# Performance work log

Measured on AMD Instinct MI355X. Metric: run time of the kernel, lower is better.

The kernel has to match this reference:

```python
import jax, jax.numpy as jnp
import numpy as np

ORDER = 2
BN_EPS = 1e-5

def setup_inputs() -> dict:
    key = jax.random.key(0)
    ks = jax.random.split(key, 8)
    B, N, L, H = 32, 512, 12, 64
    S = 2                      # support_len
    OUT = 64                   # out_dim
    M = ORDER * S * H          # einsum middle dim = 256
    x = jax.random.normal(ks[0], (B, N, L, H), dtype=jnp.float32)
    # row-scaled random diffusion matrices to keep multi-hop propagation stable
    support = jax.random.uniform(ks[1], (S, N, N), dtype=jnp.float32) / N
    scale = 1.0 / M
    weight = scale * jax.random.normal(ks[2], (L, M, OUT), dtype=jnp.float32)
    eps = jnp.zeros((1,), dtype=jnp.float32)
    gamma = jnp.ones((OUT,), dtype=jnp.float32)
    beta = jnp.zeros((OUT,), dtype=jnp.float32)
    w2 = jax.random.normal(ks[3], (OUT, OUT), dtype=jnp.float32) / np.sqrt(OUT)
    b2 = jnp.zeros((OUT,), dtype=jnp.float32)
    return {"x": x, "support": support, "weight": weight, "eps": eps,
            "gamma": gamma, "beta": beta, "w2": w2, "b2": b2}

def reference(x, support, weight, eps, gamma, beta, w2, b2):
    B, N, L, H = x.shape
    xv = x.reshape(B, N, L * H)            # [B,N,LH]
    res = []
    for i in range(support.shape[0]):      # small fixed loop over supports
        A = support[i]                     # [N,N]
        out = xv
        for _ in range(ORDER):
            out = (1.0 + eps) * out + jnp.einsum('nm,bmd->bnd', A, out)
            res.append(out)
    out = jnp.stack(res, axis=-1)          # [B,N,LH,K], K = order*support_len
    K = out.shape[-1]
    out = out.reshape(B, N, L, H * K)      # [B,N,L,M]
    out = jnp.einsum('bnlm,lmo->bno', out, weight)   # [B,N,OUT]
    # dropout is identity in eval mode
    C = out.shape[-1]
    flat = out.reshape(B * N, C)
    mean = flat.mean(axis=0)
    var = flat.var(axis=0)                 # biased, matching torch BN training
    normed = (flat - mean) * jax.lax.rsqrt(var + BN_EPS) * gamma + beta
    y = jax.nn.relu(normed.reshape(B, N, C))
    return jnp.einsum('bnc,oc->bno', y, w2) + b2
```

## Files before the change

kernel.cpp:

```cpp
#include <hip/hip_runtime.h>
#include <hip/hip_bf16.h>
#include <cstddef>
#include <cstdint>

#define B_   32
#define N_   512
#define D_   768
#define OUT_ 64
#define R_   (B_ * N_)

typedef unsigned short u16;
typedef __bf16 bf16x8 __attribute__((ext_vector_type(8)));
typedef float  f32x4  __attribute__((ext_vector_type(4)));
typedef unsigned short u16x8 __attribute__((ext_vector_type(8)));

__device__ __forceinline__ u16 f2bf(float f) {
    __hip_bfloat16 h = __float2bfloat16(f);
    return __builtin_bit_cast(u16, h);
}

__device__ __forceinline__ f32x4 mfma16(u16x8 a, u16x8 b, f32x4 c) {
    return __builtin_amdgcn_mfma_f32_16x16x32_bf16(
        __builtin_bit_cast(bf16x8, a), __builtin_bit_cast(bf16x8, b), c, 0, 0, 0);
}

__device__ __forceinline__ void gl2lds16(const void* g, void* l) {
    __builtin_amdgcn_global_load_lds(
        (const __attribute__((address_space(1))) unsigned int*)g,
        (__attribute__((address_space(3))) unsigned int*)l, 16, 0, 0);
}

__global__ __launch_bounds__(256) void cast_x(
    const float* __restrict__ x, u16* __restrict__ xb)
{
    int i = (blockIdx.x * 256 + threadIdx.x) * 8;
    f32x4 a = *(const f32x4*)(x + i);
    f32x4 b = *(const f32x4*)(x + i + 4);
    u16x8 o;
#pragma unroll
    for (int j = 0; j < 4; ++j) { o[j] = f2bf(a[j]); o[4 + j] = f2bf(b[j]); }
    *(u16x8*)(xb + i) = o;
}

__global__ __launch_bounds__(256) void build_M(
    const float* __restrict__ support, const float* __restrict__ epsp,
    u16* __restrict__ Mall, u16* __restrict__ MT)
{
    __shared__ float t[32][33];
    const int tid = threadIdx.x;
    const int s = blockIdx.z, n0 = blockIdx.y * 32, m0 = blockIdx.x * 32;
    const float f = 1.0f + epsp[0];
    const float* S = support + (size_t)s * 262144;
#pragma unroll
    for (int p = 0; p < 4; ++p) {
        int nl = p * 8 + (tid >> 5), ml = tid & 31;
        float v = S[(size_t)(n0 + nl) * 512 + m0 + ml];
        if (n0 + nl == m0 + ml) v += f;
        Mall[(size_t)s * 524288 + (size_t)(n0 + nl) * 512 + m0 + ml] = f2bf(v);
        t[nl][ml] = v;
    }
    __syncthreads();
#pragma unroll
    for (int p = 0; p < 4; ++p) {
        int ml = p * 8 + (tid >> 5), nl = tid & 31;
        MT[(size_t)s * 262144 + (size_t)(m0 + ml) * 512 + n0 + nl] = f2bf(t[nl][ml]);
    }
}

__global__ __launch_bounds__(256) void build_Wt(
    const float* __restrict__ w, u16* __restrict__ Wt)
{
    int idx = blockIdx.x * 256 + threadIdx.x;
    int k = idx / 49152, rem = idx % 49152;
    int o = rem / 768, d = rem % 768;
    int l = d >> 6, hh = d & 63;
    Wt[idx] = f2bf(w[((size_t)l * 256 + hh * 4 + k) * 64 + o]);
}

__global__ __launch_bounds__(256) void msq(
    const u16* __restrict__ Mall_in, const u16* __restrict__ MT,
    u16* __restrict__ Mall_out)
{
    __shared__ __align__(16) u16 sm[8192];
    u16* Ps = sm; u16* Qs = sm + 4096;
    const int tid = threadIdx.x, lane = tid & 63, wid = tid >> 6;
    const int wr = wid >> 1, wc = wid & 1;
    const int s = blockIdx.z, i0 = blockIdx.y * 128, j0 = blockIdx.x * 128;
    const u16* A = Mall_in + (size_t)s * 524288;
    const u16* Bq = MT + (size_t)s * 262144;
    const int lrow = lane & 15, lk = (lane >> 4) * 8;

    const u16* gsrc[4]; u16* ldst[4];
#pragma unroll
    for (int t = 0; t < 4; ++t) {
        int idx = wid * 4 + t;
        if (idx < 8) { gsrc[t] = A  + (size_t)(i0 + idx * 16 + lrow) * 512 + lk; ldst[t] = Ps + idx * 512; }
        else { int s2 = idx - 8; gsrc[t] = Bq + (size_t)(j0 + s2 * 16 + lrow) * 512 + lk; ldst[t] = Qs + s2 * 512; }
    }
    f32x4 acc[4][4] = {};
    for (int k0 = 0; k0 < 512; k0 += 32) {
#pragma unroll
        for (int t = 0; t < 4; ++t) gl2lds16(gsrc[t], ldst[t]);
#pragma unroll
        for (int t = 0; t < 4; ++t) gsrc[t] += 32;
        __syncthreads();
        u16x8 af[4], bq[4];
#pragma unroll
        for (int f = 0; f < 4; ++f) af[f] = *(const u16x8*)(Ps + (wr * 4 + f) * 512 + lane * 8);
#pragma unroll
        for (int f = 0; f < 4; ++f) bq[f] = *(const u16x8*)(Qs + (wc * 4 + f) * 512 + lane * 8);
#pragma unroll
        for (int fi = 0; fi < 4; ++fi)
#pragma unroll
            for (int fj = 0; fj < 4; ++fj) acc[fi][fj] = mfma16(af[fi], bq[fj], acc[fi][fj]);
        __syncthreads();
    }
    const int q = lane >> 4;
    u16* Co = Mall_out + (size_t)s * 524288 + 262144;
#pragma unroll
    for (int fi = 0; fi < 4; ++fi)
#pragma unroll
        for (int fj = 0; fj < 4; ++fj)
#pragma unroll
            for (int r = 0; r < 4; ++r) {
                int n = i0 + wr * 64 + fi * 16 + q * 4 + r;
                int c = j0 + wc * 64 + fj * 16 + lrow;
                Co[(size_t)n * 512 + c] = f2bf(acc[fi][fj][r]);
            }
}

__global__ __launch_bounds__(256) void zgemm(
    const u16* __restrict__ Wt, const u16* __restrict__ xb, u16* __restrict__ Z)
{
    __shared__ __align__(16) char smem[4 * 9216];
    u16* Ps = (u16*)smem;
    u16* Qs = (u16*)(smem + 8192);
    const int tid = threadIdx.x, lane = tid & 63, wid = tid >> 6;
    const int wr = wid >> 1, wc = wid & 1;
    const int j0 = blockIdx.x * 128, i0 = blockIdx.y * 128;
    const int lrow = lane & 15, lk = (lane >> 4) * 8;

    const u16* gsrc[4]; u16* ldst[4];
#pragma unroll
    for (int t = 0; t < 4; ++t) {
        int idx = wid * 4 + t;
        if (idx < 8) { gsrc[t] = Wt + (size_t)(i0 + idx * 16 + lrow) * 768 + lk; ldst[t] = Ps + idx * 512; }
        else { int s2 = idx - 8; gsrc[t] = xb + (size_t)(j0 + s2 * 16 + lrow) * 768 + lk; ldst[t] = Qs + s2 * 512; }
    }
    f32x4 acc[4][4] = {};
    for (int k0 = 0; k0 < 768; k0 += 32) {
#pragma unroll
        for (int t = 0; t < 4; ++t) gl2lds16(gsrc[t], ldst[t]);
#pragma unroll
        for (int t = 0; t < 4; ++t) gsrc[t] += 32;
        __syncthreads();
        u16x8 af[4], bq[4];
#pragma unroll
        for (int f = 0; f < 4; ++f) af[f] = *(const u16x8*)(Ps + (wr * 4 + f) * 512 + lane * 8);
#pragma unroll
        for (int f = 0; f < 4; ++f) bq[f] = *(const u16x8*)(Qs + (wc * 4 + f) * 512 + lane * 8);
#pragma unroll
        for (int fi = 0; fi < 4; ++fi)
#pragma unroll
            for (int fj = 0; fj < 4; ++fj) acc[fi][fj] = mfma16(af[fi], bq[fj], acc[fi][fj]);
        __syncthreads();
    }
    u16* Rw = (u16*)(smem + wid * 9216);
    const int q = lane >> 4;
#pragma unroll
    for (int fi = 0; fi < 4; ++fi)
#pragma unroll
        for (int fj = 0; fj < 4; ++fj)
#pragma unroll
            for (int r = 0; r < 4; ++r)
                Rw[(fi * 16 + q * 4 + r) * 72 + fj * 16 + lrow] = f2bf(acc[fi][fj][r]);
    __syncthreads();
    const int kq = blockIdx.y * 2 + wr;
    const int b  = j0 >> 9;
    const int m0 = (j0 & 511) + wc * 64;
#pragma unroll
    for (int p = 0; p < 8; ++p) {
        int row = p * 8 + (lane >> 3);
        int cc  = (lane & 7) * 8;
        u16x8 v = *(const u16x8*)(Rw + row * 72 + cc);
        *(u16x8*)(Z + ((size_t)(kq * 32 + b) * 64 + row) * 512 + m0 + cc) = v;
    }
}

__global__ __launch_bounds__(256) void ygemm(
    const u16* __restrict__ Mall, const u16* __restrict__ Z, float* __restrict__ Y1)
{
    __shared__ __align__(16) u16 sm[10240];
    u16* As_ = sm; u16* Bs_ = sm + 8192;
    const int tid = threadIdx.x, lane = tid & 63, wid = tid >> 6;
    const int n0 = blockIdx.x * 256, kb = blockIdx.y;
    const int k = kb >> 5;
    const u16* Ak  = Mall + (size_t)k * 262144;
    const u16* Zkb = Z + (size_t)kb * 64 * 512;
    const int lrow = lane & 15, lk = (lane >> 4) * 8;

    const u16* gsrc[5]; u16* ldst[5];
#pragma unroll
    for (int t = 0; t < 5; ++t) {
        int idx = wid * 5 + t;
        if (idx < 16) { gsrc[t] = Ak + (size_t)(n0 + idx * 16 + lrow) * 512 + lk; ldst[t] = As_ + idx * 512; }
        else { int s2 = idx - 16; gsrc[t] = Zkb + (size_t)(s2 * 16 + lrow) * 512 + lk; ldst[t] = Bs_ + s2 * 512; }
    }
    f32x4 acc[4][4] = {};
    for (int k0 = 0; k0 < 512; k0 += 32) {
#pragma unroll
        for (int t = 0; t < 5; ++t) gl2lds16(gsrc[t], ldst[t]);
#pragma unroll
        for (int t = 0; t < 5; ++t) gsrc[t] += 32;
        __syncthreads();
        u16x8 af[4], bq[4];
#pragma unroll
        for (int f = 0; f < 4; ++f) af[f] = *(const u16x8*)(As_ + (wid * 4 + f) * 512 + lane * 8);
#pragma unroll
        for (int f = 0; f < 4; ++f) bq[f] = *(const u16x8*)(Bs_ + f * 512 + lane * 8);
#pragma unroll
        for (int fi = 0; fi < 4; ++fi)
#pragma unroll
            for (int fj = 0; fj < 4; ++fj) acc[fi][fj] = mfma16(af[fi], bq[fj], acc[fi][fj]);
        __syncthreads();
    }
    const int q = lane >> 4;
    float* Yb = Y1 + (size_t)kb * 512 * 64;
#pragma unroll
    for (int fi = 0; fi < 4; ++fi)
#pragma unroll
        for (int fj = 0; fj < 4; ++fj)
#pragma unroll
            for (int r = 0; r < 4; ++r) {
                int n = n0 + wid * 64 + fi * 16 + q * 4 + r;
                int o = fj * 16 + lrow;
                Yb[(size_t)n * 64 + o] = acc[fi][fj][r];
            }
}

__global__ __launch_bounds__(256) void bn_part(
    const float* __restrict__ Y1, float* __restrict__ part)
{
    const int blk = blockIdx.x, tid = threadIdx.x;
    const int o = tid & 63, g = tid >> 6;
    float s = 0.f, s2 = 0.f;
    for (int r = blk * 64 + g; r < blk * 64 + 64; r += 4) {
        float v = 0.f;
#pragma unroll
        for (int k = 0; k < 4; ++k) v += Y1[((size_t)(k << 14) + r) * 64 + o];
        s += v; s2 += v * v;
    }
    __shared__ float ls[4][64], ls2[4][64];
    ls[g][o] = s; ls2[g][o] = s2;
    __syncthreads();
    if (tid < 64) {
        float t = 0.f, t2 = 0.f;
#pragma unroll
        for (int g2 = 0; g2 < 4; ++g2) { t += ls[g2][tid]; t2 += ls2[g2][tid]; }
        part[blk * 128 + tid]      = t;
        part[blk * 128 + 64 + tid] = t2;
    }
}

__global__ __launch_bounds__(256) void bn_final(
    const float* __restrict__ part, float* __restrict__ stats)
{
    const int tid = threadIdx.x;
    const int c = tid & 63, g = tid >> 6;
    float s = 0.f, s2 = 0.f;
    for (int b = g; b < 256; b += 4) {
        s  += part[b * 128 + c];
        s2 += part[b * 128 + 64 + c];
    }
    __shared__ float ls[4][64], ls2[4][64];
    ls[g][c] = s; ls2[g][c] = s2;
    __syncthreads();
    if (tid < 64) {
        float t = 0.f, t2 = 0.f;
#pragma unroll
        for (int g2 = 0; g2 < 4; ++g2) { t += ls[g2][tid]; t2 += ls2[g2][tid]; }
        float mean = t * (1.0f / R_);
        float var  = t2 * (1.0f / R_) - mean * mean;
        stats[tid]      = mean;
        stats[64 + tid] = rsqrtf(var + 1e-5f);
    }
}

__global__ __launch_bounds__(256) void bn_out(
    const float* __restrict__ Y1, const float* __restrict__ stats,
    const float* __restrict__ gamma, const float* __restrict__ beta,
    const float* __restrict__ w2, const float* __restrict__ b2,
    float* __restrict__ out)
{
    __shared__ float ys[64 * 68];
    __shared__ float w2s[64 * 65];
    __shared__ float mn[64], rs[64], ga[64], be[64], bb[64];
    const int tid = threadIdx.x;
    const int r0 = blockIdx.x * 64;
#pragma unroll
    for (int i = 0; i < 16; ++i) {
        int idx = tid + i * 256;
        w2s[(idx >> 6) * 65 + (idx & 63)] = w2[idx];
    }
    if (tid < 64) {
        mn[tid] = stats[tid]; rs[tid] = stats[64 + tid];
        ga[tid] = gamma[tid]; be[tid] = beta[tid]; bb[tid] = b2[tid];
    }
    __syncthreads();
    const int o = tid & 63, rg = tid >> 6;
#pragma unroll
    for (int p = 0; p < 16; ++p) {
        int rl = p * 4 + rg;
        int r = r0 + rl;
        float v = 0.f;
#pragma unroll
        for (int k = 0; k < 4; ++k) v += Y1[((size_t)(k << 14) + r) * 64 + o];
        v = (v - mn[o]) * rs[o] * ga[o] + be[o];
        ys[o * 68 + rl] = fmaxf(v, 0.f);
    }
    __syncthreads();
    const int ol = tid & 63, rg2 = tid >> 6;
    float acc[16];
#pragma unroll
    for (int j = 0; j < 16; ++j) acc[j] = bb[ol];
    for (int c = 0; c < 64; ++c) {
        float wv = w2s[ol * 65 + c];
        const float* yr = ys + c * 68 + rg2 * 16;
        f32x4 y0 = *(const f32x4*)(yr);
        f32x4 y1 = *(const f32x4*)(yr + 4);
        f32x4 y2 = *(const f32x4*)(yr + 8);
        f32x4 y3 = *(const f32x4*)(yr + 12);
#pragma unroll
        for (int j = 0; j < 4; ++j) {
            acc[j]      = fmaf(wv, y0[j], acc[j]);
            acc[4 + j]  = fmaf(wv, y1[j], acc[4 + j]);
            acc[8 + j]  = fmaf(wv, y2[j], acc[8 + j]);
            acc[12 + j] = fmaf(wv, y3[j], acc[12 + j]);
        }
    }
#pragma unroll
    for (int j = 0; j < 16; ++j)
        out[(size_t)(r0 + rg2 * 16 + j) * OUT_ + ol] = acc[j];
}

extern "C" void kernel_launch(void* const* d_in, const int* in_sizes, int n_in,
                              void* d_out, int out_size, void* d_ws, size_t ws_size,
                              hipStream_t stream)
{
    const float* x       = (const float*)d_in[0];
    const float* support = (const float*)d_in[1];
    const float* weight  = (const float*)d_in[2];
    const float* eps     = (const float*)d_in[3];
    const float* gamma   = (const float*)d_in[4];
    const float* beta    = (const float*)d_in[5];
    const float* w2      = (const float*)d_in[6];
    const float* b2      = (const float*)d_in[7];
    float* out = (float*)d_out;

    char* ws = (char*)d_ws;
    u16*   xb    = (u16*)(ws);
    u16*   Mall  = (u16*)(ws + 25165824);
    u16*   MT    = (u16*)(ws + 27262976);
    u16*   Wt    = (u16*)(ws + 28311552);
    u16*   Z     = (u16*)(ws + 28704768);
    float* Y1    = (float*)(ws + 37093376);
    float* part  = (float*)(ws + 53870592);
    float* stats = (float*)(ws + 54001664);

    cast_x  <<<6144,            256, 0, stream>>>(x, xb);
    build_M <<<dim3(16, 16, 2), 256, 0, stream>>>(support, eps, Mall, MT);
    build_Wt<<<768,             256, 0, stream>>>(weight, Wt);
    msq     <<<dim3(4, 4, 2),   256, 0, stream>>>(Mall, MT, Mall);
    zgemm   <<<dim3(128, 2),    256, 0, stream>>>(Wt, xb, Z);
    ygemm   <<<dim3(2, 128),    256, 0, stream>>>(Mall, Z, Y1);
    bn_part <<<256,             256, 0, stream>>>(Y1, part);
    bn_final<<<1,               256, 0, stream>>>(part, stats);
    bn_out  <<<256,             256, 0, stream>>>(Y1, stats, gamma, beta, w2, b2, out);
}
```

Before: 192.1 us.

## Fuse prep kernels, interleave M powers, and sum K terms inside Y GEMM

Merges the three preprocessing kernels into a single launch. Stores the support-power matrices in an interleaved [N, K*N] layout and the Z intermediate in [B*64, K*N], so each wave of the new ysum kernel handles one hop term. The four partial results are then reduced in LDS, which drops the 4x fp32 Y1 buffer. ysum also emits the BN partial sums, removing the bn_part kernel and the later re-read of Y1, at the cost of smaller per-wave tiles and more LDS per block.

```diff
diff --git a/kernel.cpp b/kernel.cpp
--- a/kernel.cpp
+++ b/kernel.cpp
@@ -30,72 +30,68 @@
         (__attribute__((address_space(3))) unsigned int*)l, 16, 0, 0);
 }
 
-__global__ __launch_bounds__(256) void cast_x(
-    const float* __restrict__ x, u16* __restrict__ xb)
-{
-    int i = (blockIdx.x * 256 + threadIdx.x) * 8;
-    f32x4 a = *(const f32x4*)(x + i);
-    f32x4 b = *(const f32x4*)(x + i + 4);
-    u16x8 o;
-#pragma unroll
-    for (int j = 0; j < 4; ++j) { o[j] = f2bf(a[j]); o[4 + j] = f2bf(b[j]); }
-    *(u16x8*)(xb + i) = o;
-}
-
-__global__ __launch_bounds__(256) void build_M(
-    const float* __restrict__ support, const float* __restrict__ epsp,
-    u16* __restrict__ Mall, u16* __restrict__ MT)
-{
+__global__ __launch_bounds__(256) void prep(
+    const float* __restrict__ x, const float* __restrict__ support,
+    const float* __restrict__ weight, const float* __restrict__ epsp,
+    u16* __restrict__ xb, u16* __restrict__ MallC, u16* __restrict__ MT,
+    u16* __restrict__ Wt)
+{
+    const int blk = blockIdx.x, tid = threadIdx.x;
     __shared__ float t[32][33];
-    const int tid = threadIdx.x;
-    const int s = blockIdx.z, n0 = blockIdx.y * 32, m0 = blockIdx.x * 32;
-    const float f = 1.0f + epsp[0];
-    const float* S = support + (size_t)s * 262144;
-#pragma unroll
-    for (int p = 0; p < 4; ++p) {
-        int nl = p * 8 + (tid >> 5), ml = tid & 31;
-        float v = S[(size_t)(n0 + nl) * 512 + m0 + ml];
-        if (n0 + nl == m0 + ml) v += f;
-        Mall[(size_t)s * 524288 + (size_t)(n0 + nl) * 512 + m0 + ml] = f2bf(v);
-        t[nl][ml] = v;
-    }
-    __syncthreads();
-#pragma unroll
-    for (int p = 0; p < 4; ++p) {
-        int ml = p * 8 + (tid >> 5), nl = tid & 31;
-        MT[(size_t)s * 262144 + (size_t)(m0 + ml) * 512 + n0 + nl] = f2bf(t[nl][ml]);
-    }
-}
-
-__global__ __launch_bounds__(256) void build_Wt(
-    const float* __restrict__ w, u16* __restrict__ Wt)
-{
-    int idx = blockIdx.x * 256 + threadIdx.x;
-    int k = idx / 49152, rem = idx % 49152;
-    int o = rem / 768, d = rem % 768;
-    int l = d >> 6, hh = d & 63;
-    Wt[idx] = f2bf(w[((size_t)l * 256 + hh * 4 + k) * 64 + o]);
+    if (blk < 6144) {
+        int i = (blk * 256 + tid) * 8;
+        f32x4 a = *(const f32x4*)(x + i);
+        f32x4 b = *(const f32x4*)(x + i + 4);
+        u16x8 o;
+#pragma unroll
+        for (int j = 0; j < 4; ++j) { o[j] = f2bf(a[j]); o[4 + j] = f2bf(b[j]); }
+        *(u16x8*)(xb + i) = o;
+    } else if (blk < 6656) {
+        int local = blk - 6144;
+        int s = local >> 8, rem = local & 255;
+        int n0 = (rem >> 4) * 32, m0 = (rem & 15) * 32;
+        const float f = 1.0f + epsp[0];
+        const float* S = support + (size_t)s * 262144;
+#pragma unroll
+        for (int p = 0; p < 4; ++p) {
+            int nl = p * 8 + (tid >> 5), ml = tid & 31;
+            float v = S[(size_t)(n0 + nl) * 512 + m0 + ml];
+            if (n0 + nl == m0 + ml) v += f;
+            MallC[(size_t)(n0 + nl) * 2048 + s * 1024 + m0 + ml] = f2bf(v);
+            t[nl][ml] = v;
+        }
+        __syncthreads();
+#pragma unroll
+        for (int p = 0; p < 4; ++p) {
+            int ml = p * 8 + (tid >> 5), nl = tid & 31;
+            MT[(size_t)s * 262144 + (size_t)(m0 + ml) * 512 + n0 + nl] = f2bf(t[nl][ml]);
+        }
+    } else {
+        int idx = (blk - 6656) * 256 + tid;
+        int k = idx / 49152, rem = idx % 49152;
+        int o = rem / 768, d = rem % 768;
+        int l = d >> 6, hh = d & 63;
+        Wt[idx] = f2bf(weight[((size_t)l * 256 + hh * 4 + k) * 64 + o]);
+    }
 }
 
 __global__ __launch_bounds__(256) void msq(
-    const u16* __restrict__ Mall_in, const u16* __restrict__ MT,
-    u16* __restrict__ Mall_out)
+    const u16* __restrict__ MallC_in, const u16* __restrict__ MT,
+    u16* __restrict__ MallC_out)
 {
     __shared__ __align__(16) u16 sm[8192];
     u16* Ps = sm; u16* Qs = sm + 4096;
     const int tid = threadIdx.x, lane = tid & 63, wid = tid >> 6;
     const int wr = wid >> 1, wc = wid & 1;
     const int s = blockIdx.z, i0 = blockIdx.y * 128, j0 = blockIdx.x * 128;
-    const u16* A = Mall_in + (size_t)s * 524288;
-    const u16* Bq = MT + (size_t)s * 262144;
     const int lrow = lane & 15, lk = (lane >> 4) * 8;
 
     const u16* gsrc[4]; u16* ldst[4];
 #pragma unroll
     for (int t = 0; t < 4; ++t) {
         int idx = wid * 4 + t;
-        if (idx < 8) { gsrc[t] = A  + (size_t)(i0 + idx * 16 + lrow) * 512 + lk; ldst[t] = Ps + idx * 512; }
-        else { int s2 = idx - 8; gsrc[t] = Bq + (size_t)(j0 + s2 * 16 + lrow) * 512 + lk; ldst[t] = Qs + s2 * 512; }
+        if (idx < 8) { gsrc[t] = MallC_in + (size_t)(i0 + idx * 16 + lrow) * 2048 + s * 1024 + lk; ldst[t] = Ps + idx * 512; }
+        else { int s2 = idx - 8; gsrc[t] = MT + (size_t)s * 262144 + (size_t)(j0 + s2 * 16 + lrow) * 512 + lk; ldst[t] = Qs + s2 * 512; }
     }
     f32x4 acc[4][4] = {};
     for (int k0 = 0; k0 < 512; k0 += 32) {
@@ -116,7 +112,6 @@
         __syncthreads();
     }
     const int q = lane >> 4;
-    u16* Co = Mall_out + (size_t)s * 524288 + 262144;
 #pragma unroll
     for (int fi = 0; fi < 4; ++fi)
 #pragma unroll
@@ -125,140 +120,143 @@
             for (int r = 0; r < 4; ++r) {
                 int n = i0 + wr * 64 + fi * 16 + q * 4 + r;
                 int c = j0 + wc * 64 + fj * 16 + lrow;
-                Co[(size_t)n * 512 + c] = f2bf(acc[fi][fj][r]);
+                MallC_out[(size_t)n * 2048 + (2 * s + 1) * 512 + c] = f2bf(acc[fi][fj][r]);
             }
 }
 
 __global__ __launch_bounds__(256) void zgemm(
     const u16* __restrict__ Wt, const u16* __restrict__ xb, u16* __restrict__ Z)
 {
-    __shared__ __align__(16) char smem[4 * 9216];
-    u16* Ps = (u16*)smem;
-    u16* Qs = (u16*)(smem + 8192);
+    __shared__ __align__(16) u16 sm[9216];
+    u16* As = sm; u16* Bs = sm + 2048;
     const int tid = threadIdx.x, lane = tid & 63, wid = tid >> 6;
     const int wr = wid >> 1, wc = wid & 1;
-    const int j0 = blockIdx.x * 128, i0 = blockIdx.y * 128;
+    const int j0 = blockIdx.x * 128, k = blockIdx.y;
+    const int b = j0 >> 9, m0 = j0 & 511;
     const int lrow = lane & 15, lk = (lane >> 4) * 8;
 
-    const u16* gsrc[4]; u16* ldst[4];
-#pragma unroll
-    for (int t = 0; t < 4; ++t) {
-        int idx = wid * 4 + t;
-        if (idx < 8) { gsrc[t] = Wt + (size_t)(i0 + idx * 16 + lrow) * 768 + lk; ldst[t] = Ps + idx * 512; }
-        else { int s2 = idx - 8; gsrc[t] = xb + (size_t)(j0 + s2 * 16 + lrow) * 768 + lk; ldst[t] = Qs + s2 * 512; }
-    }
-    f32x4 acc[4][4] = {};
+    const u16* gsrc[3]; u16* ldst[3];
+#pragma unroll
+    for (int t = 0; t < 3; ++t) {
+        int idx = wid * 3 + t;
+        if (idx < 4) { gsrc[t] = Wt + (size_t)(k * 64 + idx * 16 + lrow) * 768 + lk; ldst[t] = As + idx * 512; }
+        else { int s2 = idx - 4; gsrc[t] = xb + (size_t)(j0 + s2 * 16 + lrow) * 768 + lk; ldst[t] = Bs + s2 * 512; }
+    }
+    f32x4 acc[2][4] = {};
     for (int k0 = 0; k0 < 768; k0 += 32) {
 #pragma unroll
-        for (int t = 0; t < 4; ++t) gl2lds16(gsrc[t], ldst[t]);
-#pragma unroll
-        for (int t = 0; t < 4; ++t) gsrc[t] += 32;
-        __syncthreads();
-        u16x8 af[4], bq[4];
-#pragma unroll
-        for (int f = 0; f < 4; ++f) af[f] = *(const u16x8*)(Ps + (wr * 4 + f) * 512 + lane * 8);
-#pragma unroll
-        for (int f = 0; f < 4; ++f) bq[f] = *(const u16x8*)(Qs + (wc * 4 + f) * 512 + lane * 8);
-#pragma unroll
-        for (int fi = 0; fi < 4; ++fi)
+        for (int t = 0; t < 3; ++t) gl2lds16(gsrc[t], ldst[t]);
+#pragma unroll
+        for (int t = 0; t < 3; ++t) gsrc[t] += 32;
+        __syncthreads();
+        u16x8 af[2], bq[4];
+#pragma unroll
+        for (int f = 0; f < 2; ++f) af[f] = *(const u16x8*)(As + (wr * 2 + f) * 512 + lane * 8);
+#pragma unroll
+        for (int f = 0; f < 4; ++f) bq[f] = *(const u16x8*)(Bs + (wc * 4 + f) * 512 + lane * 8);
+#pragma unroll
+        for (int fi = 0; fi < 2; ++fi)
 #pragma unroll
             for (int fj = 0; fj < 4; ++fj) acc[fi][fj] = mfma16(af[fi], bq[fj], acc[fi][fj]);
         __syncthreads();
     }
-    u16* Rw = (u16*)(smem + wid * 9216);
+    u16* Rw = sm + wid * 2304;
     const int q = lane >> 4;
 #pragma unroll
-    for (int fi = 0; fi < 4; ++fi)
+    for (int fi = 0; fi < 2; ++fi)
 #pragma unroll
         for (int fj = 0; fj < 4; ++fj)
 #pragma unroll
             for (int r = 0; r < 4; ++r)
                 Rw[(fi * 16 + q * 4 + r) * 72 + fj * 16 + lrow] = f2bf(acc[fi][fj][r]);
     __syncthreads();
-    const int kq = blockIdx.y * 2 + wr;
-    const int b  = j0 >> 9;
-    const int m0 = (j0 & 511) + wc * 64;
-#pragma unroll
-    for (int p = 0; p < 8; ++p) {
+#pragma unroll
+    for (int p = 0; p < 4; ++p) {
         int row = p * 8 + (lane >> 3);
-        int cc  = (lane & 7) * 8;
+        int cc = (lane & 7) * 8;
+        int o = wr * 32 + row;
         u16x8 v = *(const u16x8*)(Rw + row * 72 + cc);
-        *(u16x8*)(Z + ((size_t)(kq * 32 + b) * 64 + row) * 512 + m0 + cc) = v;
-    }
-}
-
-__global__ __launch_bounds__(256) void ygemm(
-    const u16* __restrict__ Mall, const u16* __restrict__ Z, float* __restrict__ Y1)
-{
-    __shared__ __align__(16) u16 sm[10240];
-    u16* As_ = sm; u16* Bs_ = sm + 8192;
+        *(u16x8*)(Z + ((size_t)(b * 64 + o) * 4 + k) * 512 + m0 + wc * 64 + cc) = v;
+    }
+}
+
+__global__ __launch_bounds__(256) void ysum(
+    const u16* __restrict__ MallC, const u16* __restrict__ Z,
+    float* __restrict__ Ysum, float* __restrict__ part)
+{
+    __shared__ __align__(16) char smem[43520];
+    u16*   St = (u16*)smem;
+    float* Rk = (float*)smem;
+    float* vs = (float*)(smem + 34816);
     const int tid = threadIdx.x, lane = tid & 63, wid = tid >> 6;
-    const int n0 = blockIdx.x * 256, kb = blockIdx.y;
-    const int k = kb >> 5;
-    const u16* Ak  = Mall + (size_t)k * 262144;
-    const u16* Zkb = Z + (size_t)kb * 64 * 512;
+    const int n0 = blockIdx.x * 32, b = blockIdx.y;
     const int lrow = lane & 15, lk = (lane >> 4) * 8;
 
-    const u16* gsrc[5]; u16* ldst[5];
-#pragma unroll
-    for (int t = 0; t < 5; ++t) {
-        int idx = wid * 5 + t;
-        if (idx < 16) { gsrc[t] = Ak + (size_t)(n0 + idx * 16 + lrow) * 512 + lk; ldst[t] = As_ + idx * 512; }
-        else { int s2 = idx - 16; gsrc[t] = Zkb + (size_t)(s2 * 16 + lrow) * 512 + lk; ldst[t] = Bs_ + s2 * 512; }
-    }
-    f32x4 acc[4][4] = {};
+    const u16* gsrc[6]; u16* ldst[6];
+#pragma unroll
+    for (int t = 0; t < 2; ++t) {
+        gsrc[t] = MallC + (size_t)(n0 + t * 16 + lrow) * 2048 + wid * 512 + lk;
+        ldst[t] = St + (wid * 6 + t) * 512;
+    }
+#pragma unroll
+    for (int t = 0; t < 4; ++t) {
+        gsrc[2 + t] = Z + (size_t)(b * 64 + t * 16 + lrow) * 2048 + wid * 512 + lk;
+        ldst[2 + t] = St + (wid * 6 + 2 + t) * 512;
+    }
+    f32x4 acc[2][4] = {};
     for (int k0 = 0; k0 < 512; k0 += 32) {
 #pragma unroll
-        for (int t = 0; t < 5; ++t) gl2lds16(gsrc[t], ldst[t]);
-#pragma unroll
-        for (int t = 0; t < 5; ++t) gsrc[t] += 32;
-        __syncthreads();
-        u16x8 af[4], bq[4];
-#pragma unroll
-        for (int f = 0; f < 4; ++f) af[f] = *(const u16x8*)(As_ + (wid * 4 + f) * 512 + lane * 8);
-#pragma unroll
-        for (int f = 0; f < 4; ++f) bq[f] = *(const u16x8*)(Bs_ + f * 512 + lane * 8);
-#pragma unroll
-        for (int fi = 0; fi < 4; ++fi)
+        for (int t = 0; t < 6; ++t) gl2lds16(gsrc[t], ldst[t]);
+#pragma unroll
+        for (int t = 0; t < 6; ++t) gsrc[t] += 32;
+        __syncthreads();
+        u16x8 af[2], bq[4];
+#pragma unroll
+        for (int f = 0; f < 2; ++f) af[f] = *(const u16x8*)(St + (wid * 6 + f) * 512 + lane * 8);
+#pragma unroll
+        for (int f = 0; f < 4; ++f) bq[f] = *(const u16x8*)(St + (wid * 6 + 2 + f) * 512 + lane * 8);
+#pragma unroll
+        for (int fi = 0; fi < 2; ++fi)
 #pragma unroll
             for (int fj = 0; fj < 4; ++fj) acc[fi][fj] = mfma16(af[fi], bq[fj], acc[fi][fj]);
         __syncthreads();
     }
     const int q = lane >> 4;
-    float* Yb = Y1 + (size_t)kb * 512 * 64;
-#pragma unroll
-    for (int fi = 0; fi < 4; ++fi)
+#pragma unroll
+    for (int fi = 0; fi < 2; ++fi)
 #pragma unroll
         for (int fj = 0; fj < 4; ++fj)
 #pragma unroll
-            for (int r = 0; r < 4; ++r) {
-                int n = n0 + wid * 64 + fi * 16 + q * 4 + r;
-                int o = fj * 16 + lrow;
-                Yb[(size_t)n * 64 + o] = acc[fi][fj][r];
-            }
-}
-
-__global__ __launch_bounds__(256) void bn_part(
-    const float* __restrict__ Y1, float* __restrict__ part)
-{
-    const int blk = blockIdx.x, tid = threadIdx.x;
-    const int o = tid & 63, g = tid >> 6;
-    float s = 0.f, s2 = 0.f;
-    for (int r = blk * 64 + g; r < blk * 64 + 64; r += 4) {
-        float v = 0.f;
-#pragma unroll
-        for (int k = 0; k < 4; ++k) v += Y1[((size_t)(k << 14) + r) * 64 + o];
-        s += v; s2 += v * v;
-    }
-    __shared__ float ls[4][64], ls2[4][64];
-    ls[g][o] = s; ls2[g][o] = s2;
+            for (int r = 0; r < 4; ++r)
+                Rk[wid * 2176 + (fi * 16 + q * 4 + r) * 68 + fj * 16 + lrow] = acc[fi][fj][r];
+    __syncthreads();
+    {
+        const int r = tid >> 3, c0 = (tid & 7) * 8;
+        float v[8];
+#pragma unroll
+        for (int j = 0; j < 8; ++j) {
+            v[j] = Rk[r * 68 + c0 + j] + Rk[2176 + r * 68 + c0 + j]
+                 + Rk[4352 + r * 68 + c0 + j] + Rk[6528 + r * 68 + c0 + j];
+            vs[r * 68 + c0 + j] = v[j];
+        }
+        float* dst = Ysum + ((size_t)(b * 512 + n0 + r)) * 64 + c0;
+        f32x4 v0, v1;
+#pragma unroll
+        for (int j = 0; j < 4; ++j) { v0[j] = v[j]; v1[j] = v[4 + j]; }
+        *(f32x4*)dst = v0;
+        *(f32x4*)(dst + 4) = v1;
+    }
     __syncthreads();
     if (tid < 64) {
-        float t = 0.f, t2 = 0.f;
-#pragma unroll
-        for (int g2 = 0; g2 < 4; ++g2) { t += ls[g2][tid]; t2 += ls2[g2][tid]; }
-        part[blk * 128 + tid]      = t;
-        part[blk * 128 + 64 + tid] = t2;
+        float s = 0.f, s2 = 0.f;
+#pragma unroll
+        for (int r2 = 0; r2 < 32; ++r2) {
+            float u = vs[r2 * 68 + tid];
+            s += u; s2 += u * u;
+        }
+        int blk = blockIdx.y * 16 + blockIdx.x;
+        part[blk * 128 + tid]      = s;
+        part[blk * 128 + 64 + tid] = s2;
     }
 }
 
@@ -268,7 +266,7 @@
     const int tid = threadIdx.x;
     const int c = tid & 63, g = tid >> 6;
     float s = 0.f, s2 = 0.f;
-    for (int b = g; b < 256; b += 4) {
+    for (int b = g; b < 512; b += 4) {
         s  += part[b * 128 + c];
         s2 += part[b * 128 + 64 + c];
     }
@@ -287,7 +285,7 @@
 }
 
 __global__ __launch_bounds__(256) void bn_out(
-    const float* __restrict__ Y1, const float* __restrict__ stats,
+    const float* __restrict__ Ysum, const float* __restrict__ stats,
     const float* __restrict__ gamma, const float* __restrict__ beta,
     const float* __restrict__ w2, const float* __restrict__ b2,
     float* __restrict__ out)
@@ -311,21 +309,17 @@
 #pragma unroll
     for (int p = 0; p < 16; ++p) {
         int rl = p * 4 + rg;
-        int r = r0 + rl;
-        float v = 0.f;
-#pragma unroll
-        for (int k = 0; k < 4; ++k) v += Y1[((size_t)(k << 14) + r) * 64 + o];
+        float v = Ysum[(size_t)(r0 + rl) * 64 + o];
         v = (v - mn[o]) * rs[o] * ga[o] + be[o];
         ys[o * 68 + rl] = fmaxf(v, 0.f);
     }
     __syncthreads();
-    const int ol = tid & 63, rg2 = tid >> 6;
     float acc[16];
 #pragma unroll
-    for (int j = 0; j < 16; ++j) acc[j] = bb[ol];
+    for (int j = 0; j < 16; ++j) acc[j] = bb[o];
     for (int c = 0; c < 64; ++c) {
-        float wv = w2s[ol * 65 + c];
-        const float* yr = ys + c * 68 + rg2 * 16;
+        float wv = w2s[o * 65 + c];
+        const float* yr = ys + c * 68 + rg * 16;
         f32x4 y0 = *(const f32x4*)(yr);
         f32x4 y1 = *(const f32x4*)(yr + 4);
         f32x4 y2 = *(const f32x4*)(yr + 8);
@@ -340,7 +334,7 @@
     }
 #pragma unroll
     for (int j = 0; j < 16; ++j)
-        out[(size_t)(r0 + rg2 * 16 + j) * OUT_ + ol] = acc[j];
+        out[(size_t)(r0 + rg * 16 + j) * OUT_ + o] = acc[j];
 }
 
 extern "C" void kernel_launch(void* const* d_in, const int* in_sizes, int n_in,
@@ -359,21 +353,18 @@
 
     char* ws = (char*)d_ws;
     u16*   xb    = (u16*)(ws);
-    u16*   Mall  = (u16*)(ws + 25165824);
+    u16*   MallC = (u16*)(ws + 25165824);
     u16*   MT    = (u16*)(ws + 27262976);
     u16*   Wt    = (u16*)(ws + 28311552);
     u16*   Z     = (u16*)(ws + 28704768);
-    float* Y1    = (float*)(ws + 37093376);
-    float* part  = (float*)(ws + 53870592);
-    float* stats = (float*)(ws + 54001664);
-
-    cast_x  <<<6144,            256, 0, stream>>>(x, xb);
-    build_M <<<dim3(16, 16, 2), 256, 0, stream>>>(support, eps, Mall, MT);
-    build_Wt<<<768,             256, 0, stream>>>(weight, Wt);
-    msq     <<<dim3(4, 4, 2),   256, 0, stream>>>(Mall, MT, Mall);
-    zgemm   <<<dim3(128, 2),    256, 0, stream>>>(Wt, xb, Z);
-    ygemm   <<<dim3(2, 128),    256, 0, stream>>>(Mall, Z, Y1);
-    bn_part <<<256,             256, 0, stream>>>(Y1, part);
+    float* Ysum  = (float*)(ws + 37093376);
+    float* part  = (float*)(ws + 41287680);
+    float* stats = (float*)(ws + 41549824);
+
+    prep    <<<7424,            256, 0, stream>>>(x, support, weight, eps, xb, MallC, MT, Wt);
+    msq     <<<dim3(4, 4, 2),   256, 0, stream>>>(MallC, MT, MallC);
+    zgemm   <<<dim3(128, 4),    256, 0, stream>>>(Wt, xb, Z);
+    ysum    <<<dim3(16, 32),    256, 0, stream>>>(MallC, Z, Ysum, part);
     bn_final<<<1,               256, 0, stream>>>(part, stats);
-    bn_out  <<<256,             256, 0, stream>>>(Y1, stats, gamma, beta, w2, b2, out);
-}
+    bn_out  <<<256,             256, 0, stream>>>(Ysum, stats, gamma, beta, w2, b2, out);
+}
```

Result: slower. 199.7 us (+3.9%).
